# Performance work log

Hardware: AMD Instinct MI355X
Metric: run time of the kernel (lower is better)

The kernel has to match this reference:

```python
import jax, jax.numpy as jnp
import numpy as np
from jax import lax

B, T_IN, N, C_IN = 64, 12, 716, 2
RC = DC = 32      # residual / dilation channels
SC = 8            # skip channels
EC = 512          # end channels
OUT = 12
DIMS = 40
DAYS = 288
TOD = 288
TOPK = 100
DILS = [1, 2, 1, 2, 1, 2, 1, 2]  # blocks=4, layers=2
L = len(DILS)


def setup_inputs() -> dict:
    key = jax.random.key(0)
    ks = iter(jax.random.split(key, 64))
    n = lambda shape, s=0.1: jax.random.normal(next(ks), shape, jnp.float32) * s
    return dict(
        history_data=jax.random.uniform(next(ks), (B, T_IN, N, C_IN), jnp.float32),
        alpha=jnp.float32(-5.0),
        nodevec_p1=n((DAYS, DIMS), 1.0),
        nodevec_p2=n((N, DIMS), 1.0),
        nodevec_p3=n((N, DIMS), 1.0),
        nodevec_pk=n((DIMS, DIMS, DIMS), 1.0),
        pivweight=n((N, N), 1.0),
        start_W=n((RC, 1)), start_b=n((RC,)),
        starta_W=n((1, 1)), starta_b=n((1,)),
        filter_W=n((L, DC, RC, 1, 2)), filter_b=n((L, DC)),
        gate_W=n((L, DC, RC, 1, 2)), gate_b=n((L, DC)),
        skip_W=n((L, SC, DC)), skip_b=n((L, SC)),
        gconv_W=n((L, RC, 3 * DC)), gconv_b=n((L, RC)),
        pgconv_W=n((L, RC, 3 * RC)), pgconv_b=n((L, RC)),
        bn_gamma=jnp.ones((L, RC), jnp.float32),
        bn_beta=jnp.zeros((L, RC), jnp.float32),
        end1_W=n((EC, SC * 52)), end1_b=n((EC,)),
        end2_W=n((OUT, EC)), end2_b=n((OUT,)),
    )


def _conv1x1(x, W, b):  # x [B,C,N,T], W [O,C]
    return jnp.einsum('bcnt,oc->bont', x, W) + b[None, :, None, None]


def _gcn(x, A, W, b):
    # diffusion order 2 over one support; A [B,N,N] or [N,N]
    sub = 'bcvt,bwv->bcwt' if A.ndim == 3 else 'bcvt,wv->bcwt'
    x1 = jnp.einsum(sub, x, A)
    x2 = jnp.einsum(sub, x1, A)
    return _conv1x1(jnp.concatenate([x, x1, x2], axis=1), W, b)


def _forward(history_data, alpha, nodevec_p1, nodevec_p2, nodevec_p3, nodevec_pk,
             pivweight, start_W, start_b, starta_W, starta_b,
             filter_W, filter_b, gate_W, gate_b, skip_W, skip_b,
             gconv_W, gconv_b, pgconv_W, pgconv_b, bn_gamma, bn_beta,
             end1_W, end1_b, end2_W, end2_b):
    inputs = jnp.transpose(history_data[..., 0:1], (0, 3, 2, 1))  # [B,1,N,T]
    inputs = jnp.pad(inputs, ((0, 0), (0, 0), (0, 0), (1, 0)))    # T -> 13 = receptive field
    ind = (history_data[:, -1, 0, 1] * TOD).astype(jnp.int32) % DAYS

    x = _conv1x1(inputs, start_W, start_b)      # [B,RC,N,13]
    x_a = _conv1x1(inputs, starta_W, starta_b)  # [B,1,N,13]

    # dynamic adjacency (dgconstruct)
    adp = jnp.einsum('ai,ijk->ajk', nodevec_p1[ind], nodevec_pk)
    adp = jnp.einsum('bj,ajk->abk', nodevec_p2, adp)
    adp = jnp.einsum('ck,abk->abc', nodevec_p3, adp)
    adj = jax.nn.softmax(jax.nn.relu(adp), axis=2)  # [B,N,N]

    # pivotal adjacency (pivotalconstruct) with top-k node mask
    xs = x_a[:, 0].sum(0)                   # [N,T]
    y = xs.sum(1)[None, :]                  # [1,N]
    adjp = (xs[:, :-1] @ xs[:, 1:].T) / y   # [N,N]
    adjp = adjp * pivweight
    score = adjp.sum(0) + adjp.sum(1)
    _, idx = lax.top_k(score, TOPK)
    mask = jnp.zeros((N,), bool).at[idx].set(True)
    adj_p = jax.nn.softmax(jax.nn.relu(adjp * mask[:, None] * mask[None, :]), axis=1)  # [N,N]

    a_s = jax.nn.sigmoid(alpha)
    dn = ('NCHW', 'OIHW', 'NCHW')
    skip = None
    for i, d in enumerate(DILS):
        residual = x
        filt = jnp.tanh(
            lax.conv_general_dilated(residual, filter_W[i], (1, 1), 'VALID',
                                     rhs_dilation=(1, d), dimension_numbers=dn)
            + filter_b[i][None, :, None, None])
        gate = jax.nn.sigmoid(
            lax.conv_general_dilated(residual, gate_W[i], (1, 1), 'VALID',
                                     rhs_dilation=(1, d), dimension_numbers=dn)
            + gate_b[i][None, :, None, None])
        xg = _gcn(filt * gate, adj, gconv_W[i], gconv_b[i])  # [B,RC,N,T-d]
        # pgcn: diffusion on residual, then causal temporal crop by dilation
        xa = _gcn(residual, adj_p, pgconv_W[i], pgconv_b[i])[..., : residual.shape[3] - d]
        x = a_s * xa + (1.0 - a_s) * xg
        x = x + residual[..., -x.shape[3]:]
        s = _conv1x1(x, skip_W[i], skip_b[i])  # [B,SC,N,Ti]
        s = jnp.transpose(s, (0, 1, 3, 2)).reshape(s.shape[0], -1, s.shape[2], 1)  # [B,SC*Ti,N,1]
        skip = s if skip is None else jnp.concatenate([s, skip], axis=1)
        # BatchNorm2d, train-mode batch stats, fresh affine
        mu = x.mean(axis=(0, 2, 3), keepdims=True)
        var = x.var(axis=(0, 2, 3), keepdims=True)
        x = ((x - mu) / jnp.sqrt(var + 1e-5)) * bn_gamma[i][None, :, None, None] \
            + bn_beta[i][None, :, None, None]

    out = jax.nn.relu(skip)                         # [B,SC*52,N,1]
    out = jax.nn.relu(_conv1x1(out, end1_W, end1_b))
    out = _conv1x1(out, end2_W, end2_b)             # [B,OUT,N,1]
    return out


def reference(history_data, alpha, nodevec_p1, nodevec_p2, nodevec_p3, nodevec_pk,
              pivweight, start_W, start_b, starta_W, starta_b,
              filter_W, filter_b, gate_W, gate_b, skip_W, skip_b,
              gconv_W, gconv_b, pgconv_W, pgconv_b, bn_gamma, bn_beta,
              end1_W, end1_b, end2_W, end2_b):
    return _forward(history_data, alpha, nodevec_p1, nodevec_p2, nodevec_p3, nodevec_pk,
                    pivweight, start_W, start_b, starta_W, starta_b,
                    filter_W, filter_b, gate_W, gate_b, skip_W, skip_b,
                    gconv_W, gconv_b, pgconv_W, pgconv_b, bn_gamma, bn_beta,
                    end1_W, end1_b, end2_W, end2_b)
```

## Files before the change

kernel.cpp:

```cpp
#include <hip/hip_runtime.h>
#include <math.h>

#define NN 716
#define NSQ (716*716)
#define MAXG 9216
#define FPAD 70
typedef unsigned short bfu;
typedef __attribute__((ext_vector_type(8))) __bf16 bf16x8;
typedef __attribute__((ext_vector_type(4))) float f32x4;

__device__ __forceinline__ float b2f(bfu u){ union{unsigned int i; float f;} x; x.i = ((unsigned int)u)<<16; return x.f; }
__device__ __forceinline__ bfu f2b(float f){ union{float fv; unsigned int i;} x; x.fv = f; unsigned int r = (x.i + 0x7fffu + ((x.i>>16)&1u)) >> 16; return (bfu)r; }
__device__ __forceinline__ float sigmoidf_(float x){ return 1.f/(1.f+expf(-x)); }

__device__ __forceinline__ float fexp_(float x){
#if __has_builtin(__builtin_amdgcn_exp2f)
  return __builtin_amdgcn_exp2f(x * 1.44269504088896340736f);
#else
  return __expf(x);
#endif
}
__device__ __forceinline__ float frcp_(float x){
#if __has_builtin(__builtin_amdgcn_rcpf)
  return __builtin_amdgcn_rcpf(x);
#else
  return 1.f/x;
#endif
}
__device__ __forceinline__ float fsig_(float x){ return frcp_(1.f + fexp_(-x)); }
__device__ __forceinline__ float ftanh_(float x){
  float xc = fminf(fmaxf(x, -30.f), 30.f);
  float e = fexp_(-2.f*xc);
  return (1.f - e) * frcp_(1.f + e);
}


__global__ void k_ind(const float* __restrict__ hist, int* __restrict__ ind){
  int b = threadIdx.x; if (b >= 64) return;
  float v = hist[((b*12+11)*NN + 0)*2 + 1];
  ind[b] = ((int)(v*288.0f)) % 288;
}

__global__ void k_dg1(const float* __restrict__ p1, const float* __restrict__ pk,
                      const int* __restrict__ ind, float* __restrict__ tmp1){
  int b = blockIdx.x;
  __shared__ float p1s[40];
  if (threadIdx.x < 40) p1s[threadIdx.x] = p1[ind[b]*40 + threadIdx.x];
  __syncthreads();
  for (int jk = threadIdx.x; jk < 1600; jk += 256){
    float acc = 0.f;
    for (int i = 0; i < 40; ++i) acc += p1s[i]*pk[i*1600 + jk];
    tmp1[b*1600 + jk] = acc;
  }
}

__global__ void k_dg2(const float* __restrict__ p2, const float* __restrict__ tmp1,
                      float* __restrict__ tmp2){
  int b = blockIdx.y;
  __shared__ float ts[1600];
  for (int i = threadIdx.x; i < 1600; i += 256) ts[i] = tmp1[b*1600+i];
  __syncthreads();
  int idx = blockIdx.x*256 + threadIdx.x;
  if (idx >= NN*40) return;
  int n = idx/40, k = idx%40;
  float acc = 0.f;
  for (int j = 0; j < 40; ++j) acc += p2[n*40+j]*ts[j*40+k];
  tmp2[(long)b*NN*40 + idx] = acc;
}

__global__ void k_p3t(const float* __restrict__ p3, float* __restrict__ p3t){
  int v = blockIdx.x*256 + threadIdx.x; if (v >= NN) return;
  for (int k = 0; k < 40; ++k) p3t[k*NN + v] = p3[v*40 + k];
}

__global__ __launch_bounds__(256) void k_adjrow4s(const float* __restrict__ p3t,
    const float* __restrict__ tmp2, unsigned int* __restrict__ topA,
    int* __restrict__ cntA)
{
  int b = blockIdx.y, w0 = blockIdx.x*4, tid = threadIdx.x;
  int wave = tid >> 6, lane = tid & 63;
  __shared__ float t2s[4][40];
  __shared__ float buf[4][720];
  __shared__ float wred[4][4];
  __shared__ float rstat[4];
  __shared__ int pc[4][12];
  for (int i = tid; i < 160; i += 256){
    int r = i/40, k = i%40; int w = w0 + r;
    t2s[r][k] = (w < NN) ? tmp2[((long)b*NN + w)*40 + k] : 0.f;
  }
  __syncthreads();
  float lmax[4] = {0,0,0,0};
  for (int q = 0; q < 3; ++q){
    int v = tid + q*256;
    if (v < NN){
      float a[4] = {0,0,0,0};
      #pragma unroll 8
      for (int k = 0; k < 40; ++k){
        float pv = p3t[k*NN + v];
        #pragma unroll
        for (int r = 0; r < 4; ++r) a[r] += t2s[r][k]*pv;
      }
      #pragma unroll
      for (int r = 0; r < 4; ++r){
        float val = fmaxf(a[r], 0.f);
        buf[r][v] = val;
        lmax[r] = fmaxf(lmax[r], val);
      }
    }
  }
  #pragma unroll
  for (int r = 0; r < 4; ++r){
    float m = lmax[r];
    for (int s = 32; s > 0; s >>= 1) m = fmaxf(m, __shfl_xor(m, s, 64));
    if (lane == 0) wred[r][wave] = m;
  }
  __syncthreads();
  if (tid < 4) rstat[tid] = fmaxf(fmaxf(wred[tid][0], wred[tid][1]), fmaxf(wred[tid][2], wred[tid][3]));
  __syncthreads();
  float lsum[4] = {0,0,0,0};
  for (int q = 0; q < 3; ++q){
    int v = tid + q*256;
    if (v < NN){
      #pragma unroll
      for (int r = 0; r < 4; ++r){
        float e = fexp_(buf[r][v] - rstat[r]);
        buf[r][v] = e;
        lsum[r] += e;
      }
    }
  }
  __syncthreads();
  #pragma unroll
  for (int r = 0; r < 4; ++r){
    float s = lsum[r];
    for (int k = 32; k > 0; k >>= 1) s += __shfl_xor(s, k, 64);
    if (lane == 0) wred[r][wave] = s;
  }
  __syncthreads();
  if (tid < 4) rstat[tid] = frcp_(wred[tid][0] + wred[tid][1] + wred[tid][2] + wred[tid][3]);
  __syncthreads();
  for (int q = 0; q < 3; ++q){
    int v = tid + q*256;
    #pragma unroll
    for (int r = 0; r < 4; ++r){
      float p = (v < NN) ? buf[r][v]*rstat[r] : 0.f;
      unsigned long long m = __ballot(p >= 1e-7f);
      if (lane == 0) pc[r][q*4+wave] = __popcll(m);
    }
  }
  __syncthreads();
  for (int q = 0; q < 3; ++q){
    int v = tid + q*256;
    #pragma unroll
    for (int r = 0; r < 4; ++r){
      float p = (v < NN) ? buf[r][v]*rstat[r] : 0.f;
      bool qual = (p >= 1e-7f);
      unsigned long long m = __ballot(qual);
      int w = w0 + r;
      if (qual && w < NN){
        int base = 0, me = q*4+wave;
        for (int s = 0; s < me; ++s) base += pc[r][s];
        unsigned long long below = (lane == 0) ? 0ull : (m << (64-lane) >> (64-lane));
        int pos = base + __popcll(below);
        if (pos < 16)
          topA[((long)b*NN + w)*16 + pos] = (((unsigned)v)<<16) | (unsigned)f2b(p);
      }
    }
  }
  __syncthreads();
  if (tid < 4){
    int w = w0 + tid;
    if (w < NN){
      int tot = 0;
      for (int s = 0; s < 12; ++s) tot += pc[tid][s];
      cntA[(long)b*NN + w] = (tot < 16) ? tot : 16;
    }
  }
}

__global__ __launch_bounds__(256) void k_zgather(const bfu* __restrict__ Xg,
    const unsigned int* __restrict__ topA, const int* __restrict__ cntA,
    bfu* __restrict__ Zg, int M, long sx, long sz)
{
  __shared__ bfu rows[4][720];
  int b = blockIdx.y;
  int tid = threadIdx.x, wave = tid >> 6, lane = tid & 63;
  int m = blockIdx.x*4 + wave;
  if (m < M){
    const bfu* xr = Xg + (long)b*sx + (long)m*NN;
    #pragma unroll
    for (int q = 0; q < 12; ++q){
      int v = lane + q*64;
      if (v < NN) rows[wave][v] = xr[v];
    }
  }
  __syncthreads();
  if (m >= M) return;
  bfu* zr = Zg + (long)b*sz + (long)m*NN;
  const unsigned int* ta = topA + (long)b*NN*16;
  const int* ca = cntA + (long)b*NN;
  #pragma unroll
  for (int q = 0; q < 12; ++q){
    int w = lane + q*64;
    if (w < NN){
      int cnt = ca[w];
      const unsigned int* lst = ta + (long)w*16;
      float acc = 0.f;
      for (int j = 0; j < cnt; ++j){
        unsigned int e = lst[j];
        acc += b2f((bfu)(e & 0xffffu)) * b2f(rows[wave][e >> 16]);
      }
      zr[w] = f2b(acc);
    }
  }
}

__global__ void k_xs(const float* __restrict__ hist, const float* __restrict__ saW,
                     const float* __restrict__ sab, float* __restrict__ xs, float* __restrict__ y){
  int n = blockIdx.x, b = threadIdx.x;
  float w = saW[0], bb = sab[0];
  float ytot = 0.f;
  for (int t = 0; t < 13; ++t){
    float inp = (t == 0) ? 0.f : hist[((b*12 + (t-1))*NN + n)*2];
    float s = inp;
    for (int off = 32; off > 0; off >>= 1) s += __shfl_down(s, off, 64);
    if (b == 0){ float val = w*s + 64.f*bb; xs[n*13+t] = val; ytot += val; }
  }
  if (b == 0) y[n] = ytot;
}

__global__ void k_adjp(const float* __restrict__ xs, const float* __restrict__ y,
                       const float* __restrict__ piv, float* __restrict__ adjp){
  int i = blockIdx.y;
  __shared__ float xi[13];
  if (threadIdx.x < 13) xi[threadIdx.x] = xs[i*13+threadIdx.x];
  __syncthreads();
  int j = blockIdx.x*256 + threadIdx.x;
  if (j >= NN) return;
  float acc = 0.f;
  #pragma unroll
  for (int t = 0; t < 12; ++t) acc += xi[t]*xs[j*13+t+1];
  adjp[(long)i*NN+j] = acc / y[j] * piv[(long)i*NN+j];
}

__global__ void k_score(const float* __restrict__ adjp, float* __restrict__ score){
  int n = blockIdx.x, tid = threadIdx.x;
  float s = 0.f;
  for (int i = tid; i < NN; i += 256) s += adjp[(long)i*NN+n] + adjp[(long)n*NN+i];
  __shared__ float red[256];
  red[tid] = s; __syncthreads();
  for (int k = 128; k > 0; k >>= 1){ if (tid < k) red[tid] += red[tid+k]; __syncthreads(); }
  if (tid == 0) score[n] = red[0];
}

__global__ void k_topk(const float* __restrict__ score, int* __restrict__ mask){
  __shared__ float v[1024];
  __shared__ int ix[1024];
  int tid = threadIdx.x;
  for (int t = tid; t < 1024; t += 256){ v[t] = (t < NN) ? score[t] : -INFINITY; ix[t] = t; }
  __syncthreads();
  for (int k = 2; k <= 1024; k <<= 1){
    for (int j = k >> 1; j > 0; j >>= 1){
      for (int t = tid; t < 1024; t += 256){
        int l = t ^ j;
        if (l > t){
          bool up = ((t & k) == 0);
          bool g = (v[t] > v[l]) || (v[t] == v[l] && ix[t] < ix[l]);
          if (up ? !g : g){
            float tv = v[t]; v[t] = v[l]; v[l] = tv;
            int ti = ix[t]; ix[t] = ix[l]; ix[l] = ti;
          }
        }
      }
      __syncthreads();
    }
  }
  for (int t = tid; t < NN; t += 256) mask[t] = 0;
  __syncthreads();
  if (tid < 100) mask[ix[tid]] = 1;
}

__global__ void k_pivprep(const float* __restrict__ adjp, const int* __restrict__ mask,
                          int* __restrict__ idxk, int* __restrict__ rankv,
                          float* __restrict__ uvec, float* __restrict__ ApkT){
  __shared__ int sidx[100];
  int tid = threadIdx.x;
  if (tid == 0){
    int c = 0;
    for (int i = 0; i < NN; ++i){
      if (mask[i] && c < 100){ sidx[c] = i; idxk[c] = i; rankv[i] = c; ++c; }
      else rankv[i] = -1;
    }
  }
  __syncthreads();
  if (tid < 100){
    int i = sidx[tid];
    const float* row = adjp + (long)i*NN;
    float mx = 0.f;
    for (int k = 0; k < 100; ++k) mx = fmaxf(mx, row[sidx[k]]);
    float sum = 616.f * fexp_(-mx);
    for (int k = 0; k < 100; ++k) sum += fexp_(fmaxf(row[sidx[k]], 0.f) - mx);
    float inv = 1.f/sum;
    uvec[tid] = fexp_(-mx)*inv;
    for (int k = 0; k < 100; ++k)
      ApkT[k*100 + tid] = fexp_(fmaxf(row[sidx[k]], 0.f) - mx)*inv;
  }
}

__global__ void k_init_x(const float* __restrict__ hist, const float* __restrict__ sW,
                         const float* __restrict__ sb, bfu* __restrict__ x){
  int n = blockIdx.x*256 + threadIdx.x; if (n >= NN) return;
  int t = blockIdx.y, b = blockIdx.z;
  float inp = (t == 0) ? 0.f : hist[((b*12 + (t-1))*NN + n)*2];
  #pragma unroll
  for (int c = 0; c < 32; ++c)
    x[((long)(b*32+c)*13 + t)*NN + n] = f2b(sW[c]*inp + sb[c]);
}

__global__ void k_bnid(float* __restrict__ bnp){
  int c = threadIdx.x; if (c >= 32) return;
  bnp[c*2] = 1.f; bnp[c*2+1] = 0.f;
}

__global__ void k_bnfold(const float* __restrict__ fW, const float* __restrict__ fb,
                         const float* __restrict__ gW, const float* __restrict__ gb,
                         const float* __restrict__ bnp, bfu* __restrict__ Wcat,
                         float* __restrict__ bcat){
  int tid = threadIdx.x;
  for (int i = tid; i < 4096; i += 256){
    int row = i >> 6, k = i & 63;
    int o = row >> 1, isg = row & 1;
    int tap = k >> 5, c = k & 31;
    const float* W = isg ? gW : fW;
    Wcat[i] = f2b(W[(o*32+c)*2 + tap] * bnp[c*2]);
  }
  if (tid < 64){
    int o = tid >> 1, isg = tid & 1;
    const float* W = isg ? gW : fW;
    const float* B = isg ? gb : fb;
    float s = B[o];
    for (int c = 0; c < 32; ++c)
      s += (W[(o*32+c)*2] + W[(o*32+c)*2+1]) * bnp[c*2+1];
    bcat[tid] = s;
  }
}

__global__ void k_e1perm(const float* __restrict__ W, bfu* __restrict__ Wb){
  int i = blockIdx.x*256 + threadIdx.x;
  if (i >= 512*416) return;
  int e = i/416, kp = i%416;
  const int off2[9] = {0,96,176,248,304,352,384,408,416};
  const int soff[8] = {320,240,168,112,64,32,8,0};
  const int tpl[8]  = {12,10,9,7,6,4,3,1};
  int L = 0;
  #pragma unroll
  for (int q = 0; q < 8; ++q) if (kp >= off2[q+1]) L = q+1;
  int r = kp - off2[L]; int t = r>>3, sc = r&7;
  int k = soff[L] + sc*tpl[L] + t;
  Wb[e*416+kp] = f2b(W[e*416+k]);
}

#define LDST 44

__global__ __launch_bounds__(256) void gemm_mfma(const bfu* __restrict__ Xg,
    const bfu* __restrict__ Ag, bfu* __restrict__ Cg,
    int M, int K, long sx, long sa, long sc,
    const float* __restrict__ bias, int relu_out, int Trow, int Tcomp)
{
  int bx = gridDim.x, by = gridDim.y, nb = gridDim.z;
  int bX = blockIdx.x, bY = blockIdx.y, bZ = blockIdx.z;
  int bpb = bx*by, total = bpb*nb;
  if ((total & 7) == 0 && (nb & 7) == 0){
    int L = bX + bx*(bY + by*bZ);
    int xcd = L & 7, slot = L >> 3;
    bZ = xcd*(nb >> 3) + slot/bpb;
    int inner = slot % bpb;
    bX = inner % bx; bY = inner / bx;
  }
  const bfu* X = Xg + (long)bZ*sx;
  const bfu* A = Ag + (long)bZ*sa;
  bfu*       C = Cg + (long)bZ*sc;
  int m0 = bY*128, n0 = bX*128;
  __shared__ bfu Xs[128*LDST];
  __shared__ bfu As[128*LDST];
  int tid = threadIdx.x;
  int wave = tid >> 6, lane = tid & 63;
  int wm = (wave >> 1)*64, wn = (wave & 1)*64;
  int lr = lane & 15, lg = lane >> 4;
  f32x4 acc[4][4] = {};
  int ldr = tid >> 1, ldk = (tid & 1)*16;
  int mg = m0 + ldr, ng = n0 + ldr;
  int mrow = (Trow == Tcomp) ? mg : (mg/Tcomp)*Trow + (mg%Tcomp);
  const bfu* xrow = X + (long)mrow*K;
  const bfu* arow = A + (long)ng*K;
  for (int k0 = 0; k0 < K; k0 += 32){
    int kk = k0 + ldk;
    ushort4 z4 = {0,0,0,0};
    ushort4 x0=z4,x1=z4,x2=z4,x3=z4, a0=z4,a1=z4,a2=z4,a3=z4;
    if (mg < M){
      if (kk + 16 <= K){
        const ushort4* s = (const ushort4*)(xrow + kk);
        x0=s[0]; x1=s[1]; x2=s[2]; x3=s[3];
      } else {
        bfu tv[16];
        #pragma unroll
        for (int j=0;j<16;++j) tv[j] = (kk+j < K) ? xrow[kk+j] : (bfu)0;
        const ushort4* s = (const ushort4*)tv;
        x0=s[0]; x1=s[1]; x2=s[2]; x3=s[3];
      }
    }
    if (ng < NN){
      if (kk + 16 <= K){
        const ushort4* s = (const ushort4*)(arow + kk);
        a0=s[0]; a1=s[1]; a2=s[2]; a3=s[3];
      } else {
        bfu tv[16];
        #pragma unroll
        for (int j=0;j<16;++j) tv[j] = (kk+j < K) ? arow[kk+j] : (bfu)0;
        const ushort4* s = (const ushort4*)tv;
        a0=s[0]; a1=s[1]; a2=s[2]; a3=s[3];
      }
    }
    ushort4* xd = (ushort4*)&Xs[ldr*LDST + ldk];
    xd[0]=x0; xd[1]=x1; xd[2]=x2; xd[3]=x3;
    ushort4* ad = (ushort4*)&As[ldr*LDST + ldk];
    ad[0]=a0; ad[1]=a1; ad[2]=a2; ad[3]=a3;
    __syncthreads();
    bf16x8 af[4], bfr[4];
    #pragma unroll
    for (int i=0;i<4;++i){
      af[i]  = *(const bf16x8*)&Xs[(wm + i*16 + lr)*LDST + lg*8];
      bfr[i] = *(const bf16x8*)&As[(wn + i*16 + lr)*LDST + lg*8];
    }
    #pragma unroll
    for (int i=0;i<4;++i)
      #pragma unroll
      for (int j=0;j<4;++j)
        acc[i][j] = __builtin_amdgcn_mfma_f32_16x16x32_bf16(af[i], bfr[j], acc[i][j], 0,0,0);
    __syncthreads();
  }
  #pragma unroll
  for (int i=0;i<4;++i){
    #pragma unroll
    for (int r=0;r<4;++r){
      int m = m0 + wm + i*16 + lg*4 + r;
      if (m >= M) continue;
      float bv = bias ? bias[m] : 0.f;
      #pragma unroll
      for (int j=0;j<4;++j){
        int n = n0 + wn + j*16 + lr;
        if (n < NN){
          float v = acc[i][j][r] + bv;
          if (relu_out) v = fmaxf(v, 0.f);
          C[(long)m*NN + n] = f2b(v);
        }
      }
    }
  }
}

__global__ __launch_bounds__(256) void k_fg_mfma(const bfu* __restrict__ x,
    const bfu* __restrict__ Wcat, const float* __restrict__ bcat,
    bfu* __restrict__ fg, int T, int Tp, int d)
{
  __shared__ bfu Bsh[128*FPAD];
  __shared__ bfu Ash[64*FPAD];
  __shared__ float bsh[64];
  int tid = threadIdx.x;
  int n0 = blockIdx.x*128, t = blockIdx.y, b = blockIdx.z;
  for (int i = tid; i < 4096; i += 256){
    int row = i >> 6, k = i & 63;
    Ash[row*FPAD + k] = Wcat[i];
  }
  if (tid < 64) bsh[tid] = bcat[tid];
  #pragma unroll
  for (int i = 0; i < 8; ++i){
    int idx = tid + i*256;
    int n4 = (idx & 31)*4;
    int cc = idx >> 5;
    int c = cc & 31, tap = cc >> 5;
    long base = ((long)(b*32+c)*T + t + (tap ? d : 0))*NN + n0 + n4;
    ushort4 v = {0,0,0,0};
    if (n0 + n4 < NN) v = *(const ushort4*)(x + base);
    Bsh[(n4+0)*FPAD + cc] = v.x;
    Bsh[(n4+1)*FPAD + cc] = v.y;
    Bsh[(n4+2)*FPAD + cc] = v.z;
    Bsh[(n4+3)*FPAD + cc] = v.w;
  }
  __syncthreads();
  int wave = tid >> 6, lane = tid & 63;
  int lr = lane & 15, lg = lane >> 4;
  int rowbase = wave*16;
  bf16x8 a0 = *(const bf16x8*)&Ash[(rowbase+lr)*FPAD + lg*8];
  bf16x8 a1 = *(const bf16x8*)&Ash[(rowbase+lr)*FPAD + 32 + lg*8];
  float bf0 = bsh[rowbase + lg*4 + 0];
  float bg0 = bsh[rowbase + lg*4 + 1];
  float bf1 = bsh[rowbase + lg*4 + 2];
  float bg1 = bsh[rowbase + lg*4 + 3];
  int o0 = (rowbase >> 1) + lg*2;
  #pragma unroll
  for (int nt = 0; nt < 8; ++nt){
    bf16x8 b0 = *(const bf16x8*)&Bsh[(nt*16+lr)*FPAD + lg*8];
    bf16x8 b1 = *(const bf16x8*)&Bsh[(nt*16+lr)*FPAD + 32 + lg*8];
    f32x4 acc = {};
    acc = __builtin_amdgcn_mfma_f32_16x16x32_bf16(a0, b0, acc, 0,0,0);
    acc = __builtin_amdgcn_mfma_f32_16x16x32_bf16(a1, b1, acc, 0,0,0);
    int n = n0 + nt*16 + lr;
    if (n < NN){
      float f0 = acc[0] + bf0, g0 = acc[1] + bg0;
      float f1 = acc[2] + bf1, g1 = acc[3] + bg1;
      fg[((long)(b*32+o0)*Tp + t)*NN + n]   = f2b(ftanh_(f0)*fsig_(g0));
      fg[((long)(b*32+o0+1)*Tp + t)*NN + n] = f2b(ftanh_(f1)*fsig_(g1));
    }
  }
}

__global__ __launch_bounds__(256) void k_pgdiff1c(const bfu* __restrict__ X,
    float* __restrict__ U, bfu* __restrict__ Yk,
    const int* __restrict__ idxk, const float* __restrict__ uvec,
    const float* __restrict__ ApkT, const float* __restrict__ bnp,
    int M, int Trow, int Tcomp)
{
  __shared__ float xks[4][100];
  int tid = threadIdx.x;
  int g = tid >> 6, lane = tid & 63;
  int m = blockIdx.x*4 + g;
  bool act = (m < M);
  float s = 0.f, sk = 0.f;
  if (act){
    int mrow = (m/Tcomp)*Trow + (m%Tcomp);
    const bfu* xr = X + (long)mrow*NN;
    #pragma unroll
    for (int q = 0; q < 12; ++q){
      int v = lane + q*64;
      if (v < NN) s += b2f(xr[v]);
    }
    for (int o = 32; o; o >>= 1) s += __shfl_xor(s, o, 64);
    #pragma unroll
    for (int q = 0; q < 2; ++q){
      int k = lane + q*64;
      if (k < 100){
        float v = b2f(xr[idxk[k]]);
        xks[g][k] = v;
        sk += v;
      }
    }
    for (int o = 32; o; o >>= 1) sk += __shfl_xor(sk, o, 64);
  }
  __syncthreads();
  if (!act) return;
  int c = (m / Tcomp) & 31;
  float sb = bnp[c*2], bb = bnp[c*2+1];
  if (lane == 0) U[m] = sb*(s*(1.f/716.f)) + bb;
  #pragma unroll
  for (int q = 0; q < 2; ++q){
    int r = lane + q*64;
    if (r < 100){
      float acc = uvec[r]*(s - sk);
      for (int k = 0; k < 100; ++k) acc += ApkT[k*100 + r]*xks[g][k];
      Yk[(long)m*100 + r] = f2b(sb*acc + bb);
    }
  }
}

__global__ __launch_bounds__(256) void k_pgdiff2c(const float* __restrict__ U1,
    const bfu* __restrict__ Y1k, float* __restrict__ U2, bfu* __restrict__ Y2k,
    const float* __restrict__ uvec, const float* __restrict__ ApkT, int M)
{
  __shared__ float yks[4][100];
  int tid = threadIdx.x;
  int g = tid >> 6, lane = tid & 63;
  int m = blockIdx.x*4 + g;
  bool act = (m < M);
  float sumY = 0.f;
  if (act){
    const bfu* yr = Y1k + (long)m*100;
    #pragma unroll
    for (int q = 0; q < 2; ++q){
      int k = lane + q*64;
      if (k < 100){
        float v = b2f(yr[k]);
        yks[g][k] = v;
        sumY += v;
      }
    }
    for (int o = 32; o; o >>= 1) sumY += __shfl_xor(sumY, o, 64);
  }
  __syncthreads();
  if (!act) return;
  float base = 616.f*U1[m];
  if (lane == 0) U2[m] = (base + sumY)*(1.f/716.f);
  #pragma unroll
  for (int q = 0; q < 2; ++q){
    int r = lane + q*64;
    if (r < 100){
      float acc = uvec[r]*base;
      for (int k = 0; k < 100; ++k) acc += ApkT[k*100 + r]*yks[g][k];
      Y2k[(long)m*100 + r] = f2b(acc);
    }
  }
}

__global__ __launch_bounds__(256) void k_ymix(const float* __restrict__ U1,
    const float* __restrict__ U2, const bfu* __restrict__ Y1k, const bfu* __restrict__ Y2k,
    const float* __restrict__ pWl, float* __restrict__ V12, float* __restrict__ M12, int Tp)
{
  int t = blockIdx.x, b = blockIdx.y, tid = threadIdx.x;
  __shared__ float w1t[1024], w2t[1024];
  __shared__ float y1s[3200], y2s[3200];
  __shared__ float u1s[32], u2s[32];
  for (int i = tid; i < 1024; i += 256){
    int o = i & 31, c = i >> 5;
    w1t[c*32+o] = pWl[o*96+32+c];
    w2t[c*32+o] = pWl[o*96+64+c];
  }
  for (int i = tid; i < 3200; i += 256){
    int c = i/100, r = i - c*100;
    long m = (long)(b*32+c)*Tp + t;
    y1s[i] = b2f(Y1k[m*100 + r]);
    y2s[i] = b2f(Y2k[m*100 + r]);
  }
  if (tid < 32){
    long m = (long)(b*32+tid)*Tp + t;
    u1s[tid] = U1[m]; u2s[tid] = U2[m];
  }
  __syncthreads();
  for (int i = tid; i < 3200; i += 256){
    int r = i >> 5, o = i & 31;
    float acc = 0.f;
    #pragma unroll 8
    for (int c = 0; c < 32; ++c)
      acc += w1t[c*32+o]*y1s[c*100+r] + w2t[c*32+o]*y2s[c*100+r];
    M12[((long)(b*Tp+t)*100 + r)*32 + o] = acc;
  }
  if (tid < 32){
    float acc = 0.f;
    #pragma unroll 8
    for (int c = 0; c < 32; ++c)
      acc += w1t[c*32+tid]*u1s[c] + w2t[c*32+tid]*u2s[c];
    V12[(long)(b*Tp+t)*32 + tid] = acc;
  }
}


__global__ __launch_bounds__(256) void k_xgmix1n(bfu* __restrict__ F,
    const bfu* __restrict__ z1, const bfu* __restrict__ z2,
    const float* __restrict__ Wl, const float* __restrict__ bl,
    const float* __restrict__ alpha, int Tp)
{
  __shared__ float w0t[1024], w1t[1024], w2t[1024], bb[32];
  for (int i = threadIdx.x; i < 1024; i += 256){
    int o = i & 31, c = i >> 5;
    w0t[c*32+o] = Wl[o*96+c];
    w1t[c*32+o] = Wl[o*96+32+c];
    w2t[c*32+o] = Wl[o*96+64+c];
  }
  if (threadIdx.x < 32) bb[threadIdx.x] = bl[threadIdx.x];
  __syncthreads();
  int n = blockIdx.x*256 + threadIdx.x; if (n >= NN) return;
  int t = blockIdx.y, b = blockIdx.z;
  float acc[32];
  #pragma unroll
  for (int o = 0; o < 32; ++o) acc[o] = bb[o];
  const float4* w04 = (const float4*)w0t;
  const float4* w14 = (const float4*)w1t;
  const float4* w24 = (const float4*)w2t;
  #pragma unroll 4
  for (int c = 0; c < 32; ++c){
    long off = ((long)(b*32+c)*Tp + t)*NN + n;
    float f0 = b2f(F[off]);
    float a0 = b2f(z1[off]);
    float b0 = b2f(z2[off]);
    #pragma unroll
    for (int o4 = 0; o4 < 8; ++o4){
      float4 w0v = w04[c*8+o4], w1v = w14[c*8+o4], w2v = w24[c*8+o4];
      acc[o4*4+0] += w0v.x*f0 + w1v.x*a0 + w2v.x*b0;
      acc[o4*4+1] += w0v.y*f0 + w1v.y*a0 + w2v.y*b0;
      acc[o4*4+2] += w0v.z*f0 + w1v.z*a0 + w2v.z*b0;
      acc[o4*4+3] += w0v.w*f0 + w1v.w*a0 + w2v.w*b0;
    }
  }
  float oma = 1.f - sigmoidf_(alpha[0]);
  #pragma unroll
  for (int o = 0; o < 32; ++o)
    F[((long)(b*32+o)*Tp + t)*NN + n] = f2b(oma*acc[o]);
}

__global__ __launch_bounds__(256) void k_combine3nb(const bfu* __restrict__ x,
    bfu* __restrict__ F, const int* __restrict__ rankv,
    const float* __restrict__ M12, const float* __restrict__ V12,
    const float* __restrict__ pWl, const float* __restrict__ pbl,
    const float* __restrict__ skWl, const float* __restrict__ skbl,
    const float* __restrict__ alpha, const float* __restrict__ bnp,
    bfu* __restrict__ skipP, float* __restrict__ bnred,
    int T, int Tp, int d, int off2)
{
  __shared__ float w0t[1024];
  __shared__ float Ms[3232];
  __shared__ float swt[256], bnl[64], pbs[32], sb8[8];
  int t = blockIdx.y, b = blockIdx.z, tid = threadIdx.x;
  for (int i = tid; i < 1024; i += 256){
    int o = i & 31, c = i >> 5;
    w0t[c*32+o] = pWl[o*96+c];
  }
  for (int i = tid; i < 3232; i += 256){
    int r = i >> 5, o = i & 31;
    Ms[i] = (r < 100) ? M12[((long)(b*Tp+t)*100 + r)*32 + o]
                      : V12[(long)(b*Tp+t)*32 + o];
  }
  swt[tid] = skWl[tid];
  if (tid < 64) bnl[tid] = bnp[tid];
  if (tid < 32) pbs[tid] = pbl[tid];
  if (tid < 8)  sb8[tid] = skbl[tid];
  __syncthreads();
  int n = blockIdx.x*256 + tid;
  bool act = (n < NN);
  float acc[32];
  #pragma unroll
  for (int o = 0; o < 32; ++o) acc[o] = pbs[o];
  const float4* w04 = (const float4*)w0t;
  if (act){
    #pragma unroll 4
    for (int c = 0; c < 32; ++c){
      float sc = bnl[c*2], bc = bnl[c*2+1];
      float x0 = b2f(x[((long)(b*32+c)*T + t)*NN + n])*sc + bc;
      #pragma unroll
      for (int o4 = 0; o4 < 8; ++o4){
        float4 w = w04[c*8+o4];
        acc[o4*4+0] += w.x*x0;
        acc[o4*4+1] += w.y*x0;
        acc[o4*4+2] += w.z*x0;
        acc[o4*4+3] += w.w*x0;
      }
    }
  }
  int ra = act ? rankv[n] : -1;
  int sel = (ra < 0) ? 100 : ra;
  float a_s = sigmoidf_(alpha[0]);
  #pragma unroll
  for (int o = 0; o < 32; ++o){
    float v = 0.f;
    if (act){
      float scb = bnl[o*2], bcb = bnl[o*2+1];
      long oidx = ((long)(b*32+o)*Tp + t)*NN + n;
      float gv  = b2f(F[oidx]);
      float res = b2f(x[((long)(b*32+o)*T + t + d)*NN + n])*scb + bcb;
      v = a_s*(acc[o] + Ms[sel*32+o]) + gv + res;
      F[oidx] = f2b(v);
    }
    acc[o] = v;
  }
  {
    int wave = tid >> 6;
    int gid = ((blockIdx.x + gridDim.x*(blockIdx.y + gridDim.y*blockIdx.z)) << 2) + wave;
    #pragma unroll
    for (int o = 0; o < 32; ++o){
      float v = acc[o], vq = v*v;
      for (int s = 32; s; s >>= 1){
        v  += __shfl_xor(v,  s, 64);
        vq += __shfl_xor(vq, s, 64);
      }
      if ((tid & 63) == 0){
        bnred[((long)o*MAXG + gid)*2]     = v;
        bnred[((long)o*MAXG + gid)*2 + 1] = vq;
      }
    }
  }
  if (!act) return;
  const float4* sw4 = (const float4*)swt;
  #pragma unroll
  for (int sc2 = 0; sc2 < 8; ++sc2){
    float s0 = sb8[sc2];
    #pragma unroll
    for (int c4 = 0; c4 < 8; ++c4){
      float4 w = sw4[sc2*8 + c4];
      s0 += w.x*acc[c4*4] + w.y*acc[c4*4+1] + w.z*acc[c4*4+2] + w.w*acc[c4*4+3];
    }
    skipP[((long)b*416 + off2 + t*8 + sc2)*NN + n] = f2b(fmaxf(s0, 0.f));
  }
}

__global__ void k_bn2v2(const float* __restrict__ red, const float* __restrict__ gamma,
                        const float* __restrict__ beta, float* __restrict__ bnp,
                        int layer, int Tp, int ngroups){
  int c = blockIdx.x, tid = threadIdx.x;
  float s = 0.f, s2 = 0.f;
  for (int g = tid; g < ngroups; g += 256){
    s  += red[((long)c*MAXG + g)*2];
    s2 += red[((long)c*MAXG + g)*2 + 1];
  }
  __shared__ float rs[256], rs2[256];
  rs[tid] = s; rs2[tid] = s2; __syncthreads();
  for (int k = 128; k > 0; k >>= 1){
    if (tid < k){ rs[tid] += rs[tid+k]; rs2[tid] += rs2[tid+k]; }
    __syncthreads();
  }
  if (tid == 0){
    float cnt = 64.f*Tp*716.f;
    float mu = rs[0]/cnt, var = rs2[0]/cnt - mu*mu;
    float rstd = rsqrtf(var + 1e-5f);
    float ga = gamma[layer*32+c], be = beta[layer*32+c];
    bnp[c*2] = rstd*ga; bnp[c*2+1] = be - mu*rstd*ga;
  }
}


__global__ __launch_bounds__(256) void k_sktr(const bfu* __restrict__ SP, bfu* __restrict__ ST){
  __shared__ bfu tile[64][66];
  int b = blockIdx.z;
  int n0 = blockIdx.x*64, k0 = blockIdx.y*64;
  int tid = threadIdx.x;
  int tr = tid >> 6, tc = tid & 63;
  #pragma unroll
  for (int p = 0; p < 16; ++p){
    int k = k0 + p*4 + tr, n = n0 + tc;
    tile[p*4+tr][tc] = (k < 416 && n < NN) ? SP[((long)b*416 + k)*NN + n] : (bfu)0;
  }
  __syncthreads();
  #pragma unroll
  for (int p = 0; p < 16; ++p){
    int n = n0 + p*4 + tr, k = k0 + tc;
    if (n < NN && k < 416) ST[((long)b*NN + n)*416 + k] = tile[tc][p*4+tr];
  }
}

__global__ __launch_bounds__(256) void k_end2(const bfu* __restrict__ H,
    const float* __restrict__ W2, const float* __restrict__ b2, float* __restrict__ out)
{
  __shared__ float w[12*512];
  for (int i = threadIdx.x; i < 6144; i += 256) w[i] = W2[i];
  __syncthreads();
  int n = blockIdx.x*256 + threadIdx.x; if (n >= NN) return;
  int b = blockIdx.y;
  float acc[12];
  #pragma unroll
  for (int o = 0; o < 12; ++o) acc[o] = b2[o];
  for (int e = 0; e < 512; ++e){
    float h = b2f(H[((long)b*512+e)*NN + n]);
    #pragma unroll
    for (int o = 0; o < 12; ++o) acc[o] += w[o*512+e]*h;
  }
  #pragma unroll
  for (int o = 0; o < 12; ++o) out[((long)b*12+o)*NN + n] = acc[o];
}


extern "C" void kernel_launch(void* const* d_in, const int* in_sizes, int n_in,
                              void* d_out, int out_size, void* d_ws, size_t ws_size,
                              hipStream_t stream)
{
  const float* hist = (const float*)d_in[0];
  const float* alpha = (const float*)d_in[1];
  const float* p1  = (const float*)d_in[2];
  const float* p2  = (const float*)d_in[3];
  const float* p3  = (const float*)d_in[4];
  const float* pk  = (const float*)d_in[5];
  const float* piv = (const float*)d_in[6];
  const float* sW  = (const float*)d_in[7];
  const float* sb  = (const float*)d_in[8];
  const float* saW = (const float*)d_in[9];
  const float* sab = (const float*)d_in[10];
  const float* fW  = (const float*)d_in[11];
  const float* fb  = (const float*)d_in[12];
  const float* gW  = (const float*)d_in[13];
  const float* gb  = (const float*)d_in[14];
  const float* skW = (const float*)d_in[15];
  const float* skb = (const float*)d_in[16];
  const float* gcW = (const float*)d_in[17];
  const float* gcb = (const float*)d_in[18];
  const float* pgW = (const float*)d_in[19];
  const float* pgb = (const float*)d_in[20];
  const float* bng = (const float*)d_in[21];
  const float* bnb = (const float*)d_in[22];
  const float* e1W = (const float*)d_in[23];
  const float* e1b = (const float*)d_in[24];
  const float* e2W = (const float*)d_in[25];
  const float* e2b = (const float*)d_in[26];
  float* out = (float*)d_out;

  char* base = (char*)d_ws;
  size_t off = 0;
  auto alloc = [&](size_t bytes)->char*{
    char* r = base + off;
    off = (off + bytes + 255) & ~(size_t)255;
    return r;
  };
  const size_t SZ12 = 64UL*32*12*716*2;
  const size_t SZ13 = 64UL*32*13*716*2;
  bfu*   t1    = (bfu*)  alloc(SZ12);
  bfu*   t2    = (bfu*)  alloc(SZ12);
  bfu*   P     = (bfu*)  alloc(SZ13);
  bfu*   Q     = (bfu*)  alloc(SZ12);
  bfu*   skipP = (bfu*)  alloc(64UL*416*716*2);
  bfu*   skipT = (bfu*)  alloc(64UL*716*416*2);
  float* adjp  = (float*)alloc((size_t)NSQ*4);
  float* tmp1  = (float*)alloc(64UL*1600*4);
  float* tmp2  = (float*)alloc(64UL*716*40*4);
  float* p3t   = (float*)alloc(40UL*716*4);
  bfu*   e1Wb  = (bfu*)  alloc(512UL*416*2);
  unsigned int* topA = (unsigned int*)alloc(64UL*NN*16*4);
  int*   cntA  = (int*)  alloc(64UL*NN*4);
  bfu*   Wcat  = (bfu*)  alloc(4096UL*2);
  float* bcat  = (float*)alloc(64UL*4);
  float* xs    = (float*)alloc(716UL*13*4);
  float* yv    = (float*)alloc(716UL*4);
  float* score = (float*)alloc(716UL*4);
  float* bnred = (float*)alloc(32UL*MAXG*2*4);
  float* bnp   = (float*)alloc(64UL*4);
  float* bnpid = (float*)alloc(64UL*4);
  float* uvec  = (float*)alloc(100UL*4);
  float* ApkT  = (float*)alloc(100UL*100*4);
  int*   ind   = (int*)  alloc(64UL*4);
  int*   mask  = (int*)  alloc(716UL*4);
  int*   idxk  = (int*)  alloc(100UL*4);
  int*   rankv = (int*)  alloc(716UL*4);

  char* t1c = (char*)t1;
  float* U1  = (float*)(t1c);
  float* U2  = (float*)(t1c +   98304);
  float* V12 = (float*)(t1c + 2*98304);
  float* M12 = (float*)(t1c + 3*98304);
  bfu*   Y1k = (bfu*)  (t1c + 3*98304 + 9830400);
  bfu*   Y2k = (bfu*)  (t1c + 3*98304 + 9830400 + 4915200);

  bfu* hidden = t1;

  k_ind<<<1,64,0,stream>>>(hist, ind);
  k_dg1<<<64,256,0,stream>>>(p1, pk, ind, tmp1);
  k_dg2<<<dim3(112,64),256,0,stream>>>(p2, tmp1, tmp2);
  k_p3t<<<3,256,0,stream>>>(p3, p3t);
  k_adjrow4s<<<dim3(179,64),256,0,stream>>>(p3t, tmp2, topA, cntA);
  k_xs<<<716,64,0,stream>>>(hist, saW, sab, xs, yv);
  k_adjp<<<dim3(3,716),256,0,stream>>>(xs, yv, piv, adjp);
  k_score<<<716,256,0,stream>>>(adjp, score);
  k_topk<<<1,256,0,stream>>>(score, mask);
  k_pivprep<<<1,256,0,stream>>>(adjp, mask, idxk, rankv, uvec, ApkT);
  k_init_x<<<dim3(3,13,64),256,0,stream>>>(hist, sW, sb, P);
  k_e1perm<<<(512*416+255)/256,256,0,stream>>>(e1W, e1Wb);
  k_bnid<<<1,64,0,stream>>>(bnpid);

  int T = 13;
  bfu* x = P;
  bfu* F = Q;
  static const int off2_[8] = {0,96,176,248,304,352,384,408};
  for (int i = 0; i < 8; ++i){
    int d = (i & 1) ? 2 : 1;
    int Tp = T - d;
    const float* bnin = (i == 0) ? bnpid : bnp;
    dim3 g3(3, Tp, 64);
    k_bnfold<<<1,256,0,stream>>>(fW + i*2048, fb + i*32, gW + i*2048, gb + i*32,
        bnin, Wcat, bcat);
    k_fg_mfma<<<dim3(6,Tp,64),256,0,stream>>>(x, Wcat, bcat, F, T, Tp, d);
    int M1 = 32*Tp; long sx1 = (long)M1*NN;
    dim3 gz((M1+3)/4, 64);
    k_zgather<<<gz,256,0,stream>>>(F,  topA, cntA, t1, M1, sx1, sx1);
    k_zgather<<<gz,256,0,stream>>>(t1, topA, cntA, t2, M1, sx1, sx1);
    k_xgmix1n<<<g3,256,0,stream>>>(F, t1, t2, gcW + i*3072, gcb + i*32, alpha, Tp);
    int M2 = 64*32*Tp;
    k_pgdiff1c<<<M2/4,256,0,stream>>>(x, U1, Y1k, idxk, uvec, ApkT, bnin, M2, T, Tp);
    k_pgdiff2c<<<M2/4,256,0,stream>>>(U1, Y1k, U2, Y2k, uvec, ApkT, M2);
    k_ymix<<<dim3(Tp,64),256,0,stream>>>(U1, U2, Y1k, Y2k, pgW + i*3072, V12, M12, Tp);
    k_combine3nb<<<g3,256,0,stream>>>(x, F, rankv, M12, V12, pgW + i*3072, pgb + i*32,
        skW + i*256, skb + i*8, alpha, bnin, skipP, bnred, T, Tp, d, off2_[i]);
    int ngroups = 3*Tp*64*4;
    k_bn2v2<<<32,256,0,stream>>>(bnred, bng, bnb, bnp, i, Tp, ngroups);
    bfu* tmp = x; x = F; F = tmp;
    T = Tp;
  }
  k_sktr<<<dim3(12,7,64),256,0,stream>>>(skipP, skipT);
  gemm_mfma<<<dim3(6,4,64),256,0,stream>>>(e1Wb, skipT, hidden, 512, 416,
      0L, 416L*716, 512L*716, e1b, 1, 1, 1);
  k_end2<<<dim3(3,64),256,0,stream>>>(hidden, e2W, e2b, out);
}
```

Baseline: 2.893 ms.

## Fuse gconv mix into combine kernel and relocate pgdiff scratch buffers

Merges the k_xgmix1n 1x1 mixing of F, z1 and z2 into the combine kernel, folding the alpha scaling into shared-memory weights, biases and the M12 table. This removes one kernel launch and one bf16 write/read round trip of F per layer. The pgdiff intermediates (U1, U2, V12, M12, Y1, Y2) are moved into the skipT scratch region, presumably for locality or to reuse buffers. The Ms table is padded to a stride of 33. The fused kernel needs more shared memory and registers, which may lower occupancy, and the skipT aliasing depends on skipT being unused until after the layer loop.

Measured after the change: 2.949 ms. About the same (+1.9%).

```diff
diff --git a/kernel.cpp b/kernel.cpp
--- a/kernel.cpp
+++ b/kernel.cpp
@@ -642,110 +642,81 @@
   }
 }
 
-
-__global__ __launch_bounds__(256) void k_xgmix1n(bfu* __restrict__ F,
-    const bfu* __restrict__ z1, const bfu* __restrict__ z2,
-    const float* __restrict__ Wl, const float* __restrict__ bl,
-    const float* __restrict__ alpha, int Tp)
-{
-  __shared__ float w0t[1024], w1t[1024], w2t[1024], bb[32];
-  for (int i = threadIdx.x; i < 1024; i += 256){
-    int o = i & 31, c = i >> 5;
-    w0t[c*32+o] = Wl[o*96+c];
-    w1t[c*32+o] = Wl[o*96+32+c];
-    w2t[c*32+o] = Wl[o*96+64+c];
-  }
-  if (threadIdx.x < 32) bb[threadIdx.x] = bl[threadIdx.x];
-  __syncthreads();
-  int n = blockIdx.x*256 + threadIdx.x; if (n >= NN) return;
-  int t = blockIdx.y, b = blockIdx.z;
-  float acc[32];
-  #pragma unroll
-  for (int o = 0; o < 32; ++o) acc[o] = bb[o];
-  const float4* w04 = (const float4*)w0t;
-  const float4* w14 = (const float4*)w1t;
-  const float4* w24 = (const float4*)w2t;
-  #pragma unroll 4
-  for (int c = 0; c < 32; ++c){
-    long off = ((long)(b*32+c)*Tp + t)*NN + n;
-    float f0 = b2f(F[off]);
-    float a0 = b2f(z1[off]);
-    float b0 = b2f(z2[off]);
-    #pragma unroll
-    for (int o4 = 0; o4 < 8; ++o4){
-      float4 w0v = w04[c*8+o4], w1v = w14[c*8+o4], w2v = w24[c*8+o4];
-      acc[o4*4+0] += w0v.x*f0 + w1v.x*a0 + w2v.x*b0;
-      acc[o4*4+1] += w0v.y*f0 + w1v.y*a0 + w2v.y*b0;
-      acc[o4*4+2] += w0v.z*f0 + w1v.z*a0 + w2v.z*b0;
-      acc[o4*4+3] += w0v.w*f0 + w1v.w*a0 + w2v.w*b0;
-    }
-  }
-  float oma = 1.f - sigmoidf_(alpha[0]);
-  #pragma unroll
-  for (int o = 0; o < 32; ++o)
-    F[((long)(b*32+o)*Tp + t)*NN + n] = f2b(oma*acc[o]);
-}
-
-__global__ __launch_bounds__(256) void k_combine3nb(const bfu* __restrict__ x,
-    bfu* __restrict__ F, const int* __restrict__ rankv,
+__global__ __launch_bounds__(256) void k_fuse3(const bfu* __restrict__ x,
+    bfu* __restrict__ F, const bfu* __restrict__ z1, const bfu* __restrict__ z2,
+    const int* __restrict__ rankv,
     const float* __restrict__ M12, const float* __restrict__ V12,
+    const float* __restrict__ gcWl, const float* __restrict__ gcbl,
     const float* __restrict__ pWl, const float* __restrict__ pbl,
     const float* __restrict__ skWl, const float* __restrict__ skbl,
     const float* __restrict__ alpha, const float* __restrict__ bnp,
     bfu* __restrict__ skipP, float* __restrict__ bnred,
     int T, int Tp, int d, int off2)
 {
-  __shared__ float w0t[1024];
-  __shared__ float Ms[3232];
-  __shared__ float swt[256], bnl[64], pbs[32], sb8[8];
+  __shared__ float wx[1024], wf[1024], w1[1024], w2[1024];
+  __shared__ float Ms[101*33];
+  __shared__ float swt[256], bnl[64], base0[32], sb8[8];
   int t = blockIdx.y, b = blockIdx.z, tid = threadIdx.x;
+  float a_s = sigmoidf_(alpha[0]);
+  float oma = 1.f - a_s;
   for (int i = tid; i < 1024; i += 256){
     int o = i & 31, c = i >> 5;
-    w0t[c*32+o] = pWl[o*96+c];
-  }
-  for (int i = tid; i < 3232; i += 256){
-    int r = i >> 5, o = i & 31;
-    Ms[i] = (r < 100) ? M12[((long)(b*Tp+t)*100 + r)*32 + o]
-                      : V12[(long)(b*Tp+t)*32 + o];
+    wx[c*32+o] = a_s*pWl[o*96+c];
+    wf[c*32+o] = oma*gcWl[o*96+c];
+    w1[c*32+o] = oma*gcWl[o*96+32+c];
+    w2[c*32+o] = oma*gcWl[o*96+64+c];
+  }
+  for (int i = tid; i < 3333; i += 256){
+    int r = i/33, o = i - r*33;
+    if (o < 32)
+      Ms[r*33+o] = a_s*((r < 100) ? M12[((long)(b*Tp+t)*100 + r)*32 + o]
+                                  : V12[(long)(b*Tp+t)*32 + o]);
   }
   swt[tid] = skWl[tid];
   if (tid < 64) bnl[tid] = bnp[tid];
-  if (tid < 32) pbs[tid] = pbl[tid];
+  if (tid < 32) base0[tid] = a_s*pbl[tid] + oma*gcbl[tid];
   if (tid < 8)  sb8[tid] = skbl[tid];
   __syncthreads();
   int n = blockIdx.x*256 + tid;
   bool act = (n < NN);
   float acc[32];
   #pragma unroll
-  for (int o = 0; o < 32; ++o) acc[o] = pbs[o];
-  const float4* w04 = (const float4*)w0t;
+  for (int o = 0; o < 32; ++o) acc[o] = base0[o];
+  const float4* wx4 = (const float4*)wx;
+  const float4* wf4 = (const float4*)wf;
+  const float4* w14 = (const float4*)w1;
+  const float4* w24 = (const float4*)w2;
   if (act){
-    #pragma unroll 4
+    #pragma unroll 2
     for (int c = 0; c < 32; ++c){
       float sc = bnl[c*2], bc = bnl[c*2+1];
-      float x0 = b2f(x[((long)(b*32+c)*T + t)*NN + n])*sc + bc;
+      long offT  = ((long)(b*32+c)*T + t)*NN + n;
+      long offTp = ((long)(b*32+c)*Tp + t)*NN + n;
+      float x0 = b2f(x[offT])*sc + bc;
+      float f0 = b2f(F[offTp]);
+      float a0 = b2f(z1[offTp]);
+      float b0 = b2f(z2[offTp]);
       #pragma unroll
       for (int o4 = 0; o4 < 8; ++o4){
-        float4 w = w04[c*8+o4];
-        acc[o4*4+0] += w.x*x0;
-        acc[o4*4+1] += w.y*x0;
-        acc[o4*4+2] += w.z*x0;
-        acc[o4*4+3] += w.w*x0;
+        float4 vx = wx4[c*8+o4], vf = wf4[c*8+o4];
+        float4 v1 = w14[c*8+o4], v2 = w24[c*8+o4];
+        acc[o4*4+0] += vx.x*x0 + vf.x*f0 + v1.x*a0 + v2.x*b0;
+        acc[o4*4+1] += vx.y*x0 + vf.y*f0 + v1.y*a0 + v2.y*b0;
+        acc[o4*4+2] += vx.z*x0 + vf.z*f0 + v1.z*a0 + v2.z*b0;
+        acc[o4*4+3] += vx.w*x0 + vf.w*f0 + v1.w*a0 + v2.w*b0;
       }
     }
   }
   int ra = act ? rankv[n] : -1;
   int sel = (ra < 0) ? 100 : ra;
-  float a_s = sigmoidf_(alpha[0]);
   #pragma unroll
   for (int o = 0; o < 32; ++o){
     float v = 0.f;
     if (act){
       float scb = bnl[o*2], bcb = bnl[o*2+1];
       long oidx = ((long)(b*32+o)*Tp + t)*NN + n;
-      float gv  = b2f(F[oidx]);
       float res = b2f(x[((long)(b*32+o)*T + t + d)*NN + n])*scb + bcb;
-      v = a_s*(acc[o] + Ms[sel*32+o]) + gv + res;
+      v = acc[o] + Ms[sel*33+o] + res;
       F[oidx] = f2b(v);
     }
     acc[o] = v;
@@ -955,13 +926,22 @@
     dim3 gz((M1+3)/4, 64);
     k_zgather<<<gz,256,0,stream>>>(F,  topA, cntA, t1, M1, sx1, sx1);
     k_zgather<<<gz,256,0,stream>>>(t1, topA, cntA, t2, M1, sx1, sx1);
-    k_xgmix1n<<<g3,256,0,stream>>>(F, t1, t2, gcW + i*3072, gcb + i*32, alpha, Tp);
     int M2 = 64*32*Tp;
-    k_pgdiff1c<<<M2/4,256,0,stream>>>(x, U1, Y1k, idxk, uvec, ApkT, bnin, M2, T, Tp);
-    k_pgdiff2c<<<M2/4,256,0,stream>>>(U1, Y1k, U2, Y2k, uvec, ApkT, M2);
-    k_ymix<<<dim3(Tp,64),256,0,stream>>>(U1, U2, Y1k, Y2k, pgW + i*3072, V12, M12, Tp);
-    k_combine3nb<<<g3,256,0,stream>>>(x, F, rankv, M12, V12, pgW + i*3072, pgb + i*32,
-        skW + i*256, skb + i*8, alpha, bnin, skipP, bnred, T, Tp, d, off2_[i]);
+    {
+      char* sc2 = (char*)skipT;
+      float* U1s  = (float*)(sc2);
+      float* U2s  = (float*)(sc2 +   98304);
+      float* V12s = (float*)(sc2 + 2*98304);
+      float* M12s = (float*)(sc2 + 3*98304);
+      bfu*   Y1s  = (bfu*)  (sc2 + 3*98304 + 9830400);
+      bfu*   Y2s  = (bfu*)  (sc2 + 3*98304 + 9830400 + 4915200);
+      k_pgdiff1c<<<M2/4,256,0,stream>>>(x, U1s, Y1s, idxk, uvec, ApkT, bnin, M2, T, Tp);
+      k_pgdiff2c<<<M2/4,256,0,stream>>>(U1s, Y1s, U2s, Y2s, uvec, ApkT, M2);
+      k_ymix<<<dim3(Tp,64),256,0,stream>>>(U1s, U2s, Y1s, Y2s, pgW + i*3072, V12s, M12s, Tp);
+      k_fuse3<<<g3,256,0,stream>>>(x, F, t1, t2, rankv, M12s, V12s,
+          gcW + i*3072, gcb + i*32, pgW + i*3072, pgb + i*32,
+          skW + i*256, skb + i*8, alpha, bnin, skipP, bnred, T, Tp, d, off2_[i]);
+    }
     int ngroups = 3*Tp*64*4;
     k_bn2v2<<<32,256,0,stream>>>(bnred, bng, bnb, bnp, i, Tp, ngroups);
     bfu* tmp = x; x = F; F = tmp;
```
